# Optimization experiments

Hardware: AMD Instinct MI355X
Metric: run time of the kernel (lower is better)

## Reference

```python
import jax, jax.numpy as jnp
import numpy as np

N_NODES = 20000
N_EDGES = 320000
NF = 128   # num_node_feats
EF = 32    # num_edge_feats
CF = 3     # num_coord_feats
H = 512    # hidden_dim


def setup_inputs() -> dict:
    key = jax.random.key(0)
    ks = jax.random.split(key, 20)
    s = lambda k, shape, fan_in: jax.random.normal(k, shape, jnp.float32) / np.sqrt(fan_in)
    return {
        "hfeats": jax.random.normal(ks[0], (N_NODES, NF), jnp.float32),
        "cfeats": jax.random.normal(ks[1], (N_NODES, CF), jnp.float32),
        "efeats": jax.random.normal(ks[2], (N_EDGES, EF), jnp.float32),
        "src": jax.random.randint(ks[3], (N_EDGES,), 0, N_NODES, jnp.int32),
        "dst": jax.random.randint(ks[4], (N_EDGES,), 0, N_NODES, jnp.int32),
        # node_expansion: Linear(NF, H)
        "Wn": s(ks[5], (NF, H), NF), "bn": jnp.zeros((H,), jnp.float32),
        # edge_expansion: Linear(EF, H)
        "We": s(ks[6], (EF, H), EF), "be": jnp.zeros((H,), jnp.float32),
        # coord_expansion: Linear(CF, H)
        "Wc": s(ks[7], (CF, H), CF), "bc": jnp.zeros((H,), jnp.float32),
        # combination_reduction_nfeats: Linear(H,H) -> CELU -> Linear(H,NF) -> CELU
        "Wn1": s(ks[8], (H, H), H), "bn1": jnp.zeros((H,), jnp.float32),
        "Wn2": s(ks[9], (H, NF), H), "bn2": jnp.zeros((NF,), jnp.float32),
        # combination_reduction_efeats: Linear(H, EF) -> CELU
        "Weo": s(ks[10], (H, EF), H), "beo": jnp.zeros((EF,), jnp.float32),
        # combination_reduction_cfeats: Linear(H, CF) -> CELU
        "Wco": s(ks[11], (H, CF), H), "bco": jnp.zeros((CF,), jnp.float32),
    }


def reference(hfeats, cfeats, efeats, src, dst,
              Wn, bn, We, be, Wc, bc,
              Wn1, bn1, Wn2, bn2, Weo, beo, Wco, bco):
    celu = jax.nn.celu
    n_nodes = hfeats.shape[0]
    # Feature expansions (Linear + CELU)
    h = celu(hfeats @ Wn + bn)   # [N, H]
    e = celu(efeats @ We + be)   # [E, H]
    c = celu(cfeats @ Wc + bc)   # [N, H]
    # edge_udf: x = |c_dst - c_src| * (h_src * e)   -> [E, H]
    x = jnp.abs(c[dst] - c[src]) * (h[src] * e)
    # update_all(copy_e, sum): scatter-sum edge messages to dst nodes
    k = jax.ops.segment_sum(x, dst, num_segments=n_nodes)  # [N, H]
    # Residual combination-reductions
    h_out = hfeats + celu(celu(k @ Wn1 + bn1) @ Wn2 + bn2)
    e_out = efeats + celu(e @ Weo + beo)
    c_out = cfeats + celu(c @ Wco + bco)
    return (h_out, c_out, e_out)
```

## Files before the change

kernel.cpp:

```cpp
#include <hip/hip_runtime.h>
#include <hip/hip_bf16.h>

#define NF 128
#define EF 32
#define CF 3
#define H  512

typedef __attribute__((ext_vector_type(8))) short bf16x8;
typedef __attribute__((ext_vector_type(4))) float f32x4;

__device__ __forceinline__ float celu_f(float x) {
    return x > 0.0f ? x : __expf(x) - 1.0f;
}
__device__ __forceinline__ uint f2b(float f) {
    union { float f; uint u; } v; v.f = f;
    uint u = v.u + 0x7FFF + ((v.u >> 16) & 1);
    return u >> 16;
}
__device__ __forceinline__ float b2f(ushort s) {
    union { uint u; float f; } v; v.u = ((uint)s) << 16; return v.f;
}
__device__ __forceinline__ void unpack4(uint2 v, float* o) {
    union { uint u; float f; } x;
    x.u = v.x << 16;          o[0] = x.f;
    x.u = v.x & 0xffff0000u;  o[1] = x.f;
    x.u = v.y << 16;          o[2] = x.f;
    x.u = v.y & 0xffff0000u;  o[3] = x.f;
}

__global__ void hist_kernel(const int* __restrict__ dst, int* __restrict__ cnt, int n_edges) {
    int i = blockIdx.x * 256 + threadIdx.x;
    if (i < n_edges) atomicAdd(&cnt[dst[i]], 1);
}

__global__ void scan_kernel(int* __restrict__ cnt, int n_nodes) {
    __shared__ int part[1024];
    const int t = threadIdx.x;
    const int per = (n_nodes + 1023) / 1024;
    int s = 0;
    for (int i = 0; i < per; ++i) {
        int idx = t * per + i;
        if (idx < n_nodes) s += cnt[idx];
    }
    part[t] = s;
    __syncthreads();
    for (int off = 1; off < 1024; off <<= 1) {
        int v = (t >= off) ? part[t - off] : 0;
        __syncthreads();
        part[t] += v;
        __syncthreads();
    }
    int acc = part[t] - s;
    for (int i = 0; i < per; ++i) {
        int idx = t * per + i;
        if (idx < n_nodes) {
            int c = cnt[idx];
            cnt[idx] = acc;
            acc += c;
        }
    }
}

__global__ void scatter_kernel(const int* __restrict__ dst, int* __restrict__ cursor,
                               int* __restrict__ perm, int n_edges) {
    int i = blockIdx.x * 256 + threadIdx.x;
    if (i < n_edges) {
        int pos = atomicAdd(&cursor[dst[i]], 1);
        perm[pos] = i;
    }
}

__global__ void prep_kernel(const float* __restrict__ We, const float* __restrict__ Weo,
                            const float* __restrict__ Wn, const float* __restrict__ Wn1,
                            const float* __restrict__ Wn2,
                            ushort* __restrict__ Wet, ushort* __restrict__ Weot,
                            ushort* __restrict__ Wnt, ushort* __restrict__ Wn1t,
                            ushort* __restrict__ Wn2t) {
    int i = blockIdx.x * 256 + threadIdx.x;
    if (i < H * EF) {
        int j = i / EF, k = i % EF;
        Wet[i] = (ushort)f2b(We[(size_t)k * H + j]);
        int o = i / H, j2 = i % H;
        Weot[i] = (ushort)f2b(Weo[(size_t)j2 * EF + o]);
    }
    if (i < H * NF) {
        int o = i >> 7, k = i & 127;
        Wnt[i] = (ushort)f2b(Wn[(size_t)k * H + o]);
        int o2 = i >> 9, k2 = i & 511;
        Wn2t[i] = (ushort)f2b(Wn2[(size_t)k2 * NF + o2]);
    }
    if (i < H * H) {
        int o = i >> 9, k = i & 511;
        Wn1t[i] = (ushort)f2b(Wn1[(size_t)k * H + o]);
    }
}

__global__ __launch_bounds__(256) void node_expand_kernel(
        const float* __restrict__ hfeats, const float* __restrict__ cfeats,
        const ushort* __restrict__ Wnt, const float* __restrict__ bn,
        const float* __restrict__ Wc, const float* __restrict__ bc,
        ushort* __restrict__ hb, ushort* __restrict__ cb, int n_nodes) {
    __shared__ ushort hf[32 * NF];
    __shared__ float cf[32][4];
    const int t = threadIdx.x;
    const int lane = t & 63;
    const int w = t >> 6;
    const int node0 = blockIdx.x * 32;

    for (int i = t; i < 32 * 16; i += 256) {
        int row = i >> 4, g = i & 15;
        int node = node0 + row; if (node >= n_nodes) node = n_nodes - 1;
        const float* p = hfeats + (size_t)node * NF + g * 8;
        float4 v0 = *(const float4*)p;
        float4 v1 = *(const float4*)(p + 4);
        bf16x8 a;
        a[0] = f2b(v0.x); a[1] = f2b(v0.y); a[2] = f2b(v0.z); a[3] = f2b(v0.w);
        a[4] = f2b(v1.x); a[5] = f2b(v1.y); a[6] = f2b(v1.z); a[7] = f2b(v1.w);
        ((bf16x8*)hf)[row * 16 + (g ^ (row & 7))] = a;
    }
    for (int i = t; i < 32 * CF; i += 256) {
        int n = i / CF, k = i % CF;
        int node = node0 + n; if (node >= n_nodes) node = n_nodes - 1;
        cf[n][k] = cfeats[(size_t)node * CF + k];
    }
    __syncthreads();

    const int ar = lane & 15;
    const int hi = lane >> 4;
    const int ak = hi * 8;

    f32x4 acc[2][8];
    #pragma unroll
    for (int nt = 0; nt < 2; ++nt)
        #pragma unroll
        for (int q = 0; q < 8; ++q) { f32x4 z = {0.f,0.f,0.f,0.f}; acc[nt][q] = z; }

    for (int kstep = 0; kstep < NF / 32; ++kstep) {
        bf16x8 nfrag[2];
        #pragma unroll
        for (int nt = 0; nt < 2; ++nt) {
            int r = nt * 16 + ar;
            int g = kstep * 4 + hi;
            nfrag[nt] = ((const bf16x8*)hf)[r * 16 + (g ^ (r & 7))];
        }
        #pragma unroll
        for (int q = 0; q < 8; ++q) {
            bf16x8 wf = *(const bf16x8*)(Wnt + (size_t)((w * 8 + q) * 16 + ar) * NF + kstep * 32 + ak);
            acc[0][q] = __builtin_amdgcn_mfma_f32_16x16x32_bf16(wf, nfrag[0], acc[0][q], 0, 0, 0);
            acc[1][q] = __builtin_amdgcn_mfma_f32_16x16x32_bf16(wf, nfrag[1], acc[1][q], 0, 0, 0);
        }
    }
    #pragma unroll
    for (int q = 0; q < 8; ++q) {
        const int jbase = (w * 8 + q) * 16 + hi * 4;
        const float4 bv = *(const float4*)(bn + jbase);
        #pragma unroll
        for (int nt = 0; nt < 2; ++nt) {
            int node = node0 + nt * 16 + ar;
            if (node < n_nodes) {
                float v0 = celu_f(acc[nt][q][0] + bv.x);
                float v1 = celu_f(acc[nt][q][1] + bv.y);
                float v2 = celu_f(acc[nt][q][2] + bv.z);
                float v3 = celu_f(acc[nt][q][3] + bv.w);
                uint2 pk;
                pk.x = f2b(v0) | (f2b(v1) << 16);
                pk.y = f2b(v2) | (f2b(v3) << 16);
                *(uint2*)(hb + (size_t)node * H + jbase) = pk;
            }
        }
    }

    for (int i = t; i < 32 * 64; i += 256) {
        int n = i >> 6, gj = i & 63;
        int node = node0 + n;
        if (node < n_nodes) {
            int j = gj * 8;
            float c0 = cf[n][0], c1 = cf[n][1], c2 = cf[n][2];
            float v[8];
            #pragma unroll
            for (int u = 0; u < 8; ++u)
                v[u] = celu_f(bc[j + u] + c0 * Wc[j + u] + c1 * Wc[H + j + u] + c2 * Wc[2 * H + j + u]);
            uint4 pk;
            pk.x = f2b(v[0]) | (f2b(v[1]) << 16);
            pk.y = f2b(v[2]) | (f2b(v[3]) << 16);
            pk.z = f2b(v[4]) | (f2b(v[5]) << 16);
            pk.w = f2b(v[6]) | (f2b(v[7]) << 16);
            *(uint4*)(cb + (size_t)node * H + j) = pk;
        }
    }
}

__global__ __launch_bounds__(256) void c_out_kernel(
        const float* __restrict__ cfeats, const ushort* __restrict__ cb,
        const float* __restrict__ Wco, const float* __restrict__ bco,
        float* __restrict__ c_out, int n_nodes) {
    const int t = threadIdx.x;
    const int lane = t & 63;
    const int w = t >> 6;
    const int node = blockIdx.x * 4 + w;
    if (node >= n_nodes) return;
    float a0 = 0.f, a1 = 0.f, a2 = 0.f;
    bf16x8 v = ((const bf16x8*)(cb + (size_t)node * H))[lane];
    #pragma unroll
    for (int u = 0; u < 8; ++u) {
        int j = lane * 8 + u;
        float cv = b2f((ushort)v[u]);
        a0 += cv * Wco[j * CF + 0];
        a1 += cv * Wco[j * CF + 1];
        a2 += cv * Wco[j * CF + 2];
    }
    #pragma unroll
    for (int m = 32; m >= 1; m >>= 1) {
        a0 += __shfl_xor(a0, m);
        a1 += __shfl_xor(a1, m);
        a2 += __shfl_xor(a2, m);
    }
    if (lane < 3) {
        float s = (lane == 0) ? a0 : (lane == 1) ? a1 : a2;
        c_out[(size_t)node * CF + lane] = cfeats[(size_t)node * CF + lane] + celu_f(bco[lane] + s);
    }
}

__global__ __launch_bounds__(256) void edge_kernel(
        const float* __restrict__ efeats,
        const int* __restrict__ src, const int* __restrict__ dst,
        const int* __restrict__ perm,
        const ushort* __restrict__ Wet, const float* __restrict__ be,
        const ushort* __restrict__ Weot, const float* __restrict__ beo,
        const ushort* __restrict__ hb, const ushort* __restrict__ cb,
        float* __restrict__ k_acc, float* __restrict__ e_out, int n_edges) {
    __shared__ ushort e512[32 * 512];
    __shared__ int s_perm[32], s_src[32], s_dst[32];
    const int t = threadIdx.x;
    const int lane = t & 63;
    const int w = t >> 6;

    const int nwg = gridDim.x;
    const int q = nwg >> 3, r = nwg & 7;
    const int xcd = blockIdx.x & 7, sub = blockIdx.x >> 3;
    const int bid = (xcd < r ? xcd * (q + 1) : r * (q + 1) + (xcd - r) * q) + sub;
    const int e0 = bid * 32;

    if (t < 32) {
        int e = e0 + t;
        int pe = (e < n_edges) ? perm[e] : -1;
        s_perm[t] = pe;
        s_src[t] = (pe >= 0) ? src[pe] : 0;
        s_dst[t] = (pe >= 0) ? dst[pe] : -1;
    }
    __syncthreads();

    const int ar = lane & 15;
    const int hi = lane >> 4;
    const int ak = hi * 8;

    bf16x8 efrag[2];
    #pragma unroll
    for (int et = 0; et < 2; ++et) {
        int pe = s_perm[et * 16 + ar];
        if (pe < 0) pe = 0;
        const float* p = efeats + (size_t)pe * EF + ak;
        float4 v0 = *(const float4*)p;
        float4 v1 = *(const float4*)(p + 4);
        bf16x8 a;
        a[0] = f2b(v0.x); a[1] = f2b(v0.y); a[2] = f2b(v0.z); a[3] = f2b(v0.w);
        a[4] = f2b(v1.x); a[5] = f2b(v1.y); a[6] = f2b(v1.z); a[7] = f2b(v1.w);
        efrag[et] = a;
    }
    bf16x8 wfrag[8];
    #pragma unroll
    for (int qq = 0; qq < 8; ++qq)
        wfrag[qq] = *(const bf16x8*)(Wet + (size_t)((w * 8 + qq) * 16 + ar) * EF + ak);
    f32x4 acc[2][8];
    #pragma unroll
    for (int et = 0; et < 2; ++et)
        #pragma unroll
        for (int qq = 0; qq < 8; ++qq) { f32x4 z = {0.f,0.f,0.f,0.f}; acc[et][qq] = z; }
    #pragma unroll
    for (int qq = 0; qq < 8; ++qq) {
        acc[0][qq] = __builtin_amdgcn_mfma_f32_16x16x32_bf16(wfrag[qq], efrag[0], acc[0][qq], 0, 0, 0);
        acc[1][qq] = __builtin_amdgcn_mfma_f32_16x16x32_bf16(wfrag[qq], efrag[1], acc[1][qq], 0, 0, 0);
    }
    #pragma unroll
    for (int qq = 0; qq < 8; ++qq) {
        const int jbase = (w * 8 + qq) * 16 + hi * 4;
        const float4 bv = *(const float4*)(be + jbase);
        #pragma unroll
        for (int et = 0; et < 2; ++et) {
            const int e_l = et * 16 + ar;
            float v0 = celu_f(acc[et][qq][0] + bv.x);
            float v1 = celu_f(acc[et][qq][1] + bv.y);
            float v2 = celu_f(acc[et][qq][2] + bv.z);
            float v3 = celu_f(acc[et][qq][3] + bv.w);
            uint2 pk;
            pk.x = f2b(v0) | (f2b(v1) << 16);
            pk.y = f2b(v2) | (f2b(v3) << 16);
            const int gs = (jbase >> 3) ^ (e_l & 7);
            *(uint2*)(&e512[e_l * 512 + gs * 8 + (jbase & 7)]) = pk;
        }
    }
    __syncthreads();

    {
        const int grp = t >> 7;
        const int ct = t & 127;
        const int j0 = ct * 4;
        const int g = j0 >> 3, go = j0 & 7;
        float a_[4];
        a_[0] = a_[1] = a_[2] = a_[3] = 0.f;
        int cur = -1;
        #pragma unroll
        for (int i = 0; i < 16; ++i) {
            const int e = grp * 16 + i;
            const int d = __builtin_amdgcn_readfirstlane(s_dst[e]);
            const int dc = (d < 0) ? 0 : d;
            const int s_ = s_src[e];
            uint2 hv = *(const uint2*)(hb + (size_t)s_ * H + j0);
            uint2 sv = *(const uint2*)(cb + (size_t)s_ * H + j0);
            uint2 cv = *(const uint2*)(cb + (size_t)dc * H + j0);
            uint2 ev = *(const uint2*)(&e512[e * 512 + (g ^ (e & 7)) * 8 + go]);
            if (d != cur) {
                if (cur >= 0) {
                    #pragma unroll
                    for (int u = 0; u < 4; ++u)
                        atomicAdd(&k_acc[(size_t)cur * H + j0 + u], a_[u]);
                    a_[0] = a_[1] = a_[2] = a_[3] = 0.f;
                }
                cur = d;
            }
            if (d >= 0) {
                float hs_[4], cs_[4], cd_[4], ev_[4];
                unpack4(hv, hs_);
                unpack4(sv, cs_);
                unpack4(cv, cd_);
                unpack4(ev, ev_);
                #pragma unroll
                for (int u = 0; u < 4; ++u)
                    a_[u] += fabsf(cd_[u] - cs_[u]) * (hs_[u] * ev_[u]);
            }
        }
        if (cur >= 0) {
            #pragma unroll
            for (int u = 0; u < 4; ++u)
                atomicAdd(&k_acc[(size_t)cur * H + j0 + u], a_[u]);
        }
    }

    {
        const int ot = w & 1, et = w >> 1;
        bf16x8 wfragC[16];
        #pragma unroll
        for (int kt = 0; kt < 16; ++kt)
            wfragC[kt] = *(const bf16x8*)(Weot + (size_t)(ot * 16 + ar) * H + kt * 32 + ak);
        f32x4 accc = {0.f, 0.f, 0.f, 0.f};
        const int e_l = et * 16 + ar;
        #pragma unroll
        for (int kt = 0; kt < 16; ++kt) {
            const int gs = (kt * 4 + hi) ^ (ar & 7);
            bf16x8 b = *(const bf16x8*)(&e512[e_l * 512 + gs * 8]);
            accc = __builtin_amdgcn_mfma_f32_16x16x32_bf16(wfragC[kt], b, accc, 0, 0, 0);
        }
        const int pe = s_perm[e_l];
        if (pe >= 0) {
            const int obase = ot * 16 + hi * 4;
            const float4 bo = *(const float4*)(beo + obase);
            size_t idx = (size_t)pe * EF + obase;
            float4 ef4 = *(const float4*)(efeats + idx);
            float4 o;
            o.x = ef4.x + celu_f(accc[0] + bo.x);
            o.y = ef4.y + celu_f(accc[1] + bo.y);
            o.z = ef4.z + celu_f(accc[2] + bo.z);
            o.w = ef4.w + celu_f(accc[3] + bo.w);
            *(float4*)(e_out + idx) = o;
        }
    }
}

__global__ __launch_bounds__(256) void node_out_kernel(
        const float* __restrict__ hfeats, const float* __restrict__ k_acc,
        const ushort* __restrict__ Wn1t, const float* __restrict__ bn1,
        const ushort* __restrict__ Wn2t, const float* __restrict__ bn2,
        float* __restrict__ h_out, int n_nodes) {
    __shared__ ushort kt_s[32 * H];
    const int t = threadIdx.x;
    const int lane = t & 63;
    const int w = t >> 6;
    const int node0 = blockIdx.x * 32;

    for (int i = t; i < 32 * 64; i += 256) {
        int row = i >> 6, g = i & 63;
        int node = node0 + row; if (node >= n_nodes) node = n_nodes - 1;
        const float* p = k_acc + (size_t)node * H + g * 8;
        float4 v0 = *(const float4*)p;
        float4 v1 = *(const float4*)(p + 4);
        bf16x8 a;
        a[0] = f2b(v0.x); a[1] = f2b(v0.y); a[2] = f2b(v0.z); a[3] = f2b(v0.w);
        a[4] = f2b(v1.x); a[5] = f2b(v1.y); a[6] = f2b(v1.z); a[7] = f2b(v1.w);
        ((bf16x8*)kt_s)[row * 64 + (g ^ (row & 7))] = a;
    }
    __syncthreads();

    const int ar = lane & 15;
    const int hi = lane >> 4;
    const int ak = hi * 8;

    f32x4 acc[2][8];
    #pragma unroll
    for (int nt = 0; nt < 2; ++nt)
        #pragma unroll
        for (int q = 0; q < 8; ++q) { f32x4 z = {0.f,0.f,0.f,0.f}; acc[nt][q] = z; }

    for (int kstep = 0; kstep < H / 32; ++kstep) {
        bf16x8 kfrag[2];
        #pragma unroll
        for (int nt = 0; nt < 2; ++nt) {
            int rr = nt * 16 + ar;
            int g = kstep * 4 + hi;
            kfrag[nt] = ((const bf16x8*)kt_s)[rr * 64 + (g ^ (rr & 7))];
        }
        #pragma unroll
        for (int q = 0; q < 8; ++q) {
            bf16x8 wf = *(const bf16x8*)(Wn1t + (size_t)((w * 8 + q) * 16 + ar) * H + kstep * 32 + ak);
            acc[0][q] = __builtin_amdgcn_mfma_f32_16x16x32_bf16(wf, kfrag[0], acc[0][q], 0, 0, 0);
            acc[1][q] = __builtin_amdgcn_mfma_f32_16x16x32_bf16(wf, kfrag[1], acc[1][q], 0, 0, 0);
        }
    }
    __syncthreads();

    #pragma unroll
    for (int q = 0; q < 8; ++q) {
        const int jbase = (w * 8 + q) * 16 + hi * 4;
        const float4 bv = *(const float4*)(bn1 + jbase);
        #pragma unroll
        for (int nt = 0; nt < 2; ++nt) {
            const int rr = nt * 16 + ar;
            float v0 = celu_f(acc[nt][q][0] + bv.x);
            float v1 = celu_f(acc[nt][q][1] + bv.y);
            float v2 = celu_f(acc[nt][q][2] + bv.z);
            float v3 = celu_f(acc[nt][q][3] + bv.w);
            uint2 pk;
            pk.x = f2b(v0) | (f2b(v1) << 16);
            pk.y = f2b(v2) | (f2b(v3) << 16);
            const int gs = (jbase >> 3) ^ (rr & 7);
            *(uint2*)(&kt_s[rr * 512 + gs * 8 + (jbase & 7)]) = pk;
        }
    }
    __syncthreads();

    f32x4 acc2[2][2];
    #pragma unroll
    for (int nt = 0; nt < 2; ++nt)
        #pragma unroll
        for (int ct = 0; ct < 2; ++ct) { f32x4 z = {0.f,0.f,0.f,0.f}; acc2[nt][ct] = z; }

    for (int kstep = 0; kstep < H / 32; ++kstep) {
        bf16x8 tfrag[2];
        #pragma unroll
        for (int nt = 0; nt < 2; ++nt) {
            int rr = nt * 16 + ar;
            int g = kstep * 4 + hi;
            tfrag[nt] = ((const bf16x8*)kt_s)[rr * 64 + (g ^ (rr & 7))];
        }
        #pragma unroll
        for (int ct = 0; ct < 2; ++ct) {
            bf16x8 wf = *(const bf16x8*)(Wn2t + (size_t)((w * 2 + ct) * 16 + ar) * H + kstep * 32 + ak);
            acc2[0][ct] = __builtin_amdgcn_mfma_f32_16x16x32_bf16(wf, tfrag[0], acc2[0][ct], 0, 0, 0);
            acc2[1][ct] = __builtin_amdgcn_mfma_f32_16x16x32_bf16(wf, tfrag[1], acc2[1][ct], 0, 0, 0);
        }
    }
    #pragma unroll
    for (int ct = 0; ct < 2; ++ct) {
        const int jbase = (w * 2 + ct) * 16 + hi * 4;
        const float4 bv = *(const float4*)(bn2 + jbase);
        #pragma unroll
        for (int nt = 0; nt < 2; ++nt) {
            const int node = node0 + nt * 16 + ar;
            if (node < n_nodes) {
                size_t idx = (size_t)node * NF + jbase;
                float4 hf4 = *(const float4*)(hfeats + idx);
                float4 o;
                o.x = hf4.x + celu_f(acc2[nt][ct][0] + bv.x);
                o.y = hf4.y + celu_f(acc2[nt][ct][1] + bv.y);
                o.z = hf4.z + celu_f(acc2[nt][ct][2] + bv.z);
                o.w = hf4.w + celu_f(acc2[nt][ct][3] + bv.w);
                *(float4*)(h_out + idx) = o;
            }
        }
    }
}

extern "C" void kernel_launch(void* const* d_in, const int* in_sizes, int n_in,
                              void* d_out, int out_size, void* d_ws, size_t ws_size,
                              hipStream_t stream) {
    const float* hfeats = (const float*)d_in[0];
    const float* cfeats = (const float*)d_in[1];
    const float* efeats = (const float*)d_in[2];
    const int*   src    = (const int*)d_in[3];
    const int*   dst    = (const int*)d_in[4];
    const float* Wn  = (const float*)d_in[5];  const float* bn  = (const float*)d_in[6];
    const float* We  = (const float*)d_in[7];  const float* be  = (const float*)d_in[8];
    const float* Wc  = (const float*)d_in[9];  const float* bc  = (const float*)d_in[10];
    const float* Wn1 = (const float*)d_in[11]; const float* bn1 = (const float*)d_in[12];
    const float* Wn2 = (const float*)d_in[13]; const float* bn2 = (const float*)d_in[14];
    const float* Weo = (const float*)d_in[15]; const float* beo = (const float*)d_in[16];
    const float* Wco = (const float*)d_in[17]; const float* bco = (const float*)d_in[18];

    const int n_nodes = in_sizes[0] / NF;
    const int n_edges = in_sizes[2] / EF;

    float*  k_buf = (float*)d_ws;
    ushort* hb    = (ushort*)(k_buf + (size_t)n_nodes * H);
    ushort* cb    = hb + (size_t)n_nodes * H;
    ushort* Wet   = cb + (size_t)n_nodes * H;
    ushort* Weot  = Wet + (size_t)H * EF;
    ushort* Wnt   = Weot + (size_t)H * EF;
    ushort* Wn1t  = Wnt + (size_t)H * NF;
    ushort* Wn2t  = Wn1t + (size_t)H * H;
    int*    cnt   = (int*)(Wn2t + (size_t)NF * H);
    int*    perm  = cnt + n_nodes;

    float* h_out = (float*)d_out;
    float* c_out = h_out + (size_t)n_nodes * NF;
    float* e_out = c_out + (size_t)n_nodes * CF;

    hipMemsetAsync(k_buf, 0, (size_t)n_nodes * H * sizeof(float), stream);
    hipMemsetAsync(cnt, 0, (size_t)n_nodes * sizeof(int), stream);

    prep_kernel<<<(H * H + 255) / 256, 256, 0, stream>>>(
        We, Weo, Wn, Wn1, Wn2, Wet, Weot, Wnt, Wn1t, Wn2t);
    hist_kernel<<<(n_edges + 255) / 256, 256, 0, stream>>>(dst, cnt, n_edges);
    scan_kernel<<<1, 1024, 0, stream>>>(cnt, n_nodes);
    scatter_kernel<<<(n_edges + 255) / 256, 256, 0, stream>>>(dst, cnt, perm, n_edges);

    node_expand_kernel<<<(n_nodes + 31) / 32, 256, 0, stream>>>(
        hfeats, cfeats, Wnt, bn, Wc, bc, hb, cb, n_nodes);

    c_out_kernel<<<(n_nodes + 3) / 4, 256, 0, stream>>>(
        cfeats, cb, Wco, bco, c_out, n_nodes);

    edge_kernel<<<(n_edges + 31) / 32, 256, 0, stream>>>(
        efeats, src, dst, perm, Wet, be, Weot, beo, hb, cb, k_buf, e_out, n_edges);

    node_out_kernel<<<(n_nodes + 31) / 32, 256, 0, stream>>>(
        hfeats, k_buf, Wn1t, bn1, Wn2t, bn2, h_out, n_nodes);
}
```

Baseline: 489.4 us.

## Halve edge tile to 16 edges and use hardware bf16 packed convert

Edge kernel block tile shrinks from 32 to 16 edges. This halves shared memory and accumulator registers per block and doubles the grid, which should raise occupancy. The output projection now uses only two waves. All software round-to-nearest bf16 conversions are replaced with the v_cvt_pk_bf16_f32 instruction, and CELU is made branchless with fmax/fmin. Risks include more blocks re-reading weight fragments, idle waves in the e_out stage, and smaller scatter runs per destination node.

New measurement: 570.6 us. +16.6%, slower.

```diff
diff --git a/kernel.cpp b/kernel.cpp
--- a/kernel.cpp
+++ b/kernel.cpp
@@ -5,17 +5,24 @@
 #define EF 32
 #define CF 3
 #define H  512
+#define EB 16
 
 typedef __attribute__((ext_vector_type(8))) short bf16x8;
 typedef __attribute__((ext_vector_type(4))) float f32x4;
 
 __device__ __forceinline__ float celu_f(float x) {
-    return x > 0.0f ? x : __expf(x) - 1.0f;
-}
-__device__ __forceinline__ uint f2b(float f) {
-    union { float f; uint u; } v; v.f = f;
-    uint u = v.u + 0x7FFF + ((v.u >> 16) & 1);
-    return u >> 16;
+    return fmaxf(x, __expf(fminf(x, 0.0f)) - 1.0f);
+}
+__device__ __forceinline__ uint cvtpk(float lo, float hi) {
+    uint r;
+    asm("v_cvt_pk_bf16_f32 %0, %1, %2" : "=v"(r) : "v"(lo), "v"(hi));
+    return r;
+}
+__device__ __forceinline__ bf16x8 pack8(float4 v0, float4 v1) {
+    union { uint4 u; bf16x8 b; } r;
+    r.u.x = cvtpk(v0.x, v0.y); r.u.y = cvtpk(v0.z, v0.w);
+    r.u.z = cvtpk(v1.x, v1.y); r.u.w = cvtpk(v1.z, v1.w);
+    return r.b;
 }
 __device__ __forceinline__ float b2f(ushort s) {
     union { uint u; float f; } v; v.u = ((uint)s) << 16; return v.f;
@@ -79,19 +86,19 @@
     int i = blockIdx.x * 256 + threadIdx.x;
     if (i < H * EF) {
         int j = i / EF, k = i % EF;
-        Wet[i] = (ushort)f2b(We[(size_t)k * H + j]);
+        Wet[i] = (ushort)cvtpk(We[(size_t)k * H + j], 0.f);
         int o = i / H, j2 = i % H;
-        Weot[i] = (ushort)f2b(Weo[(size_t)j2 * EF + o]);
+        Weot[i] = (ushort)cvtpk(Weo[(size_t)j2 * EF + o], 0.f);
     }
     if (i < H * NF) {
         int o = i >> 7, k = i & 127;
-        Wnt[i] = (ushort)f2b(Wn[(size_t)k * H + o]);
+        Wnt[i] = (ushort)cvtpk(Wn[(size_t)k * H + o], 0.f);
         int o2 = i >> 9, k2 = i & 511;
-        Wn2t[i] = (ushort)f2b(Wn2[(size_t)k2 * NF + o2]);
+        Wn2t[i] = (ushort)cvtpk(Wn2[(size_t)k2 * NF + o2], 0.f);
     }
     if (i < H * H) {
         int o = i >> 9, k = i & 511;
-        Wn1t[i] = (ushort)f2b(Wn1[(size_t)k * H + o]);
+        Wn1t[i] = (ushort)cvtpk(Wn1[(size_t)k * H + o], 0.f);
     }
 }
 
@@ -113,10 +120,7 @@
         const float* p = hfeats + (size_t)node * NF + g * 8;
         float4 v0 = *(const float4*)p;
         float4 v1 = *(const float4*)(p + 4);
-        bf16x8 a;
-        a[0] = f2b(v0.x); a[1] = f2b(v0.y); a[2] = f2b(v0.z); a[3] = f2b(v0.w);
-        a[4] = f2b(v1.x); a[5] = f2b(v1.y); a[6] = f2b(v1.z); a[7] = f2b(v1.w);
-        ((bf16x8*)hf)[row * 16 + (g ^ (row & 7))] = a;
+        ((bf16x8*)hf)[row * 16 + (g ^ (row & 7))] = pack8(v0, v1);
     }
     for (int i = t; i < 32 * CF; i += 256) {
         int n = i / CF, k = i % CF;
@@ -158,13 +162,9 @@
         for (int nt = 0; nt < 2; ++nt) {
             int node = node0 + nt * 16 + ar;
             if (node < n_nodes) {
-                float v0 = celu_f(acc[nt][q][0] + bv.x);
-                float v1 = celu_f(acc[nt][q][1] + bv.y);
-                float v2 = celu_f(acc[nt][q][2] + bv.z);
-                float v3 = celu_f(acc[nt][q][3] + bv.w);
                 uint2 pk;
-                pk.x = f2b(v0) | (f2b(v1) << 16);
-                pk.y = f2b(v2) | (f2b(v3) << 16);
+                pk.x = cvtpk(celu_f(acc[nt][q][0] + bv.x), celu_f(acc[nt][q][1] + bv.y));
+                pk.y = cvtpk(celu_f(acc[nt][q][2] + bv.z), celu_f(acc[nt][q][3] + bv.w));
                 *(uint2*)(hb + (size_t)node * H + jbase) = pk;
             }
         }
@@ -181,10 +181,10 @@
             for (int u = 0; u < 8; ++u)
                 v[u] = celu_f(bc[j + u] + c0 * Wc[j + u] + c1 * Wc[H + j + u] + c2 * Wc[2 * H + j + u]);
             uint4 pk;
-            pk.x = f2b(v[0]) | (f2b(v[1]) << 16);
-            pk.y = f2b(v[2]) | (f2b(v[3]) << 16);
-            pk.z = f2b(v[4]) | (f2b(v[5]) << 16);
-            pk.w = f2b(v[6]) | (f2b(v[7]) << 16);
+            pk.x = cvtpk(v[0], v[1]);
+            pk.y = cvtpk(v[2], v[3]);
+            pk.z = cvtpk(v[4], v[5]);
+            pk.w = cvtpk(v[6], v[7]);
             *(uint4*)(cb + (size_t)node * H + j) = pk;
         }
     }
@@ -229,8 +229,8 @@
         const ushort* __restrict__ Weot, const float* __restrict__ beo,
         const ushort* __restrict__ hb, const ushort* __restrict__ cb,
         float* __restrict__ k_acc, float* __restrict__ e_out, int n_edges) {
-    __shared__ ushort e512[32 * 512];
-    __shared__ int s_perm[32], s_src[32], s_dst[32];
+    __shared__ ushort e512[EB * 512];
+    __shared__ int s_perm[EB], s_src[EB], s_dst[EB];
     const int t = threadIdx.x;
     const int lane = t & 63;
     const int w = t >> 6;
@@ -239,9 +239,9 @@
     const int q = nwg >> 3, r = nwg & 7;
     const int xcd = blockIdx.x & 7, sub = blockIdx.x >> 3;
     const int bid = (xcd < r ? xcd * (q + 1) : r * (q + 1) + (xcd - r) * q) + sub;
-    const int e0 = bid * 32;
-
-    if (t < 32) {
+    const int e0 = bid * EB;
+
+    if (t < EB) {
         int e = e0 + t;
         int pe = (e < n_edges) ? perm[e] : -1;
         s_perm[t] = pe;
@@ -254,50 +254,35 @@
     const int hi = lane >> 4;
     const int ak = hi * 8;
 
-    bf16x8 efrag[2];
-    #pragma unroll
-    for (int et = 0; et < 2; ++et) {
-        int pe = s_perm[et * 16 + ar];
+    bf16x8 efrag;
+    {
+        int pe = s_perm[ar];
         if (pe < 0) pe = 0;
         const float* p = efeats + (size_t)pe * EF + ak;
         float4 v0 = *(const float4*)p;
         float4 v1 = *(const float4*)(p + 4);
-        bf16x8 a;
-        a[0] = f2b(v0.x); a[1] = f2b(v0.y); a[2] = f2b(v0.z); a[3] = f2b(v0.w);
-        a[4] = f2b(v1.x); a[5] = f2b(v1.y); a[6] = f2b(v1.z); a[7] = f2b(v1.w);
-        efrag[et] = a;
+        efrag = pack8(v0, v1);
     }
     bf16x8 wfrag[8];
     #pragma unroll
     for (int qq = 0; qq < 8; ++qq)
         wfrag[qq] = *(const bf16x8*)(Wet + (size_t)((w * 8 + qq) * 16 + ar) * EF + ak);
-    f32x4 acc[2][8];
-    #pragma unroll
-    for (int et = 0; et < 2; ++et)
-        #pragma unroll
-        for (int qq = 0; qq < 8; ++qq) { f32x4 z = {0.f,0.f,0.f,0.f}; acc[et][qq] = z; }
-    #pragma unroll
-    for (int qq = 0; qq < 8; ++qq) {
-        acc[0][qq] = __builtin_amdgcn_mfma_f32_16x16x32_bf16(wfrag[qq], efrag[0], acc[0][qq], 0, 0, 0);
-        acc[1][qq] = __builtin_amdgcn_mfma_f32_16x16x32_bf16(wfrag[qq], efrag[1], acc[1][qq], 0, 0, 0);
-    }
+    f32x4 acc[8];
+    #pragma unroll
+    for (int qq = 0; qq < 8; ++qq) { f32x4 z = {0.f,0.f,0.f,0.f}; acc[qq] = z; }
+    #pragma unroll
+    for (int qq = 0; qq < 8; ++qq)
+        acc[qq] = __builtin_amdgcn_mfma_f32_16x16x32_bf16(wfrag[qq], efrag, acc[qq], 0, 0, 0);
     #pragma unroll
     for (int qq = 0; qq < 8; ++qq) {
         const int jbase = (w * 8 + qq) * 16 + hi * 4;
         const float4 bv = *(const float4*)(be + jbase);
-        #pragma unroll
-        for (int et = 0; et < 2; ++et) {
-            const int e_l = et * 16 + ar;
-            float v0 = celu_f(acc[et][qq][0] + bv.x);
-            float v1 = celu_f(acc[et][qq][1] + bv.y);
-            float v2 = celu_f(acc[et][qq][2] + bv.z);
-            float v3 = celu_f(acc[et][qq][3] + bv.w);
-            uint2 pk;
-            pk.x = f2b(v0) | (f2b(v1) << 16);
-            pk.y = f2b(v2) | (f2b(v3) << 16);
-            const int gs = (jbase >> 3) ^ (e_l & 7);
-            *(uint2*)(&e512[e_l * 512 + gs * 8 + (jbase & 7)]) = pk;
-        }
+        const int e_l = ar;
+        uint2 pk;
+        pk.x = cvtpk(celu_f(acc[qq][0] + bv.x), celu_f(acc[qq][1] + bv.y));
+        pk.y = cvtpk(celu_f(acc[qq][2] + bv.z), celu_f(acc[qq][3] + bv.w));
+        const int gs = (jbase >> 3) ^ (e_l & 7);
+        *(uint2*)(&e512[e_l * 512 + gs * 8 + (jbase & 7)]) = pk;
     }
     __syncthreads();
 
@@ -310,8 +295,8 @@
         a_[0] = a_[1] = a_[2] = a_[3] = 0.f;
         int cur = -1;
         #pragma unroll
-        for (int i = 0; i < 16; ++i) {
-            const int e = grp * 16 + i;
+        for (int i = 0; i < 8; ++i) {
+            const int e = grp * 8 + i;
             const int d = __builtin_amdgcn_readfirstlane(s_dst[e]);
             const int dc = (d < 0) ? 0 : d;
             const int s_ = s_src[e];
@@ -346,17 +331,17 @@
         }
     }
 
-    {
-        const int ot = w & 1, et = w >> 1;
+    if (w < 2) {
+        const int ot = w;
         bf16x8 wfragC[16];
         #pragma unroll
         for (int kt = 0; kt < 16; ++kt)
             wfragC[kt] = *(const bf16x8*)(Weot + (size_t)(ot * 16 + ar) * H + kt * 32 + ak);
         f32x4 accc = {0.f, 0.f, 0.f, 0.f};
-        const int e_l = et * 16 + ar;
+        const int e_l = ar;
         #pragma unroll
         for (int kt = 0; kt < 16; ++kt) {
-            const int gs = (kt * 4 + hi) ^ (ar & 7);
+            const int gs = (kt * 4 + hi) ^ (e_l & 7);
             bf16x8 b = *(const bf16x8*)(&e512[e_l * 512 + gs * 8]);
             accc = __builtin_amdgcn_mfma_f32_16x16x32_bf16(wfragC[kt], b, accc, 0, 0, 0);
         }
@@ -393,10 +378,7 @@
         const float* p = k_acc + (size_t)node * H + g * 8;
         float4 v0 = *(const float4*)p;
         float4 v1 = *(const float4*)(p + 4);
-        bf16x8 a;
-        a[0] = f2b(v0.x); a[1] = f2b(v0.y); a[2] = f2b(v0.z); a[3] = f2b(v0.w);
-        a[4] = f2b(v1.x); a[5] = f2b(v1.y); a[6] = f2b(v1.z); a[7] = f2b(v1.w);
-        ((bf16x8*)kt_s)[row * 64 + (g ^ (row & 7))] = a;
+        ((bf16x8*)kt_s)[row * 64 + (g ^ (row & 7))] = pack8(v0, v1);
     }
     __syncthreads();
 
@@ -434,13 +416,9 @@
         #pragma unroll
         for (int nt = 0; nt < 2; ++nt) {
             const int rr = nt * 16 + ar;
-            float v0 = celu_f(acc[nt][q][0] + bv.x);
-            float v1 = celu_f(acc[nt][q][1] + bv.y);
-            float v2 = celu_f(acc[nt][q][2] + bv.z);
-            float v3 = celu_f(acc[nt][q][3] + bv.w);
             uint2 pk;
-            pk.x = f2b(v0) | (f2b(v1) << 16);
-            pk.y = f2b(v2) | (f2b(v3) << 16);
+            pk.x = cvtpk(celu_f(acc[nt][q][0] + bv.x), celu_f(acc[nt][q][1] + bv.y));
+            pk.y = cvtpk(celu_f(acc[nt][q][2] + bv.z), celu_f(acc[nt][q][3] + bv.w));
             const int gs = (jbase >> 3) ^ (rr & 7);
             *(uint2*)(&kt_s[rr * 512 + gs * 8 + (jbase & 7)]) = pk;
         }
@@ -538,7 +516,7 @@
     c_out_kernel<<<(n_nodes + 3) / 4, 256, 0, stream>>>(
         cfeats, cb, Wco, bco, c_out, n_nodes);
 
-    edge_kernel<<<(n_edges + 31) / 32, 256, 0, stream>>>(
+    edge_kernel<<<(n_edges + EB - 1) / EB, 256, 0, stream>>>(
         efeats, src, dst, perm, Wet, be, Weot, beo, hb, cb, k_buf, e_out, n_edges);
 
     node_out_kernel<<<(n_nodes + 31) / 32, 256, 0, stream>>>(
```
